# Kernel tuning notes

Measured on AMD Instinct MI355X. Metric: run time of the kernel, lower is better.

## Reference

```python
import jax, jax.numpy as jnp
import numpy as np
import math

NUM_HEADS = 16  # power of two -> simple ALiBi slope formula

def alibi_slopes(num_heads: int) -> jnp.ndarray:
    # num_heads is a power of two here; general formula per Press et al. 2022
    k = 1 << (num_heads.bit_length() - 1)
    ratio = 2.0 ** (-8.0 / k)
    slopes = ratio ** np.arange(1, 1 + k)
    if num_heads != k:
        ratio2 = 2.0 ** (-8.0 / (2 * k))
        rest = (ratio2 ** np.arange(1, 1 + 2 * k, 2))[: num_heads - k]
        slopes = np.concatenate([slopes, rest])
    return jnp.asarray(slopes, dtype=jnp.float32).reshape(1, -1, 1, 1)


def setup_inputs() -> dict:
    key = jax.random.key(0)
    kq, kk, kv, km = jax.random.split(key, 4)
    B, H, S, D = 1, NUM_HEADS, 2048, 64
    query = jax.random.normal(kq, (B, H, S, D), dtype=jnp.float32)
    k_ = jax.random.normal(kk, (B, H, S, D), dtype=jnp.float32)
    value = jax.random.normal(kv, (B, H, S, D), dtype=jnp.float32)
    # padding-style boolean mask [B, S]; keep position 0 always valid
    mask = jax.random.randint(km, (B, S), 0, 2).astype(bool)
    mask = mask.at[:, 0].set(True)
    return {"query": query, "key": k_, "value": value, "mask": mask}


def reference(query, key, value, mask):
    B, H, S, D = query.shape
    scale = 1.0 / math.sqrt(D)
    # scores: [B, H, Sq, Sk]
    scores = jnp.einsum("bhqd,bhkd->bhqk", query, key) * scale
    # causal ALiBi bias: distances arange(1-S, 1) -> shape (1, H, 1, S)
    distances = jnp.arange(1 - S, 1, dtype=jnp.float32)
    bias = distances[None, None, None, :] * alibi_slopes(H)
    scores = scores + bias
    # boolean padding mask [B, S] -> [B, 1, 1, S]
    blocked = jnp.finfo(scores.dtype).min
    scores = jnp.where(mask[:, None, None, :], scores, blocked)
    weights = jax.nn.softmax(scores, axis=-1)
    # dropout_prob = 0.0 (eval) -> identity
    return jnp.einsum("bhqk,bhkd->bhqd", weights, value)
```

## Files before the change

kernel.cpp:

```cpp
#include <hip/hip_runtime.h>


constexpr int   S_LEN  = 2048;
constexpr int   D_DIM  = 64;
constexpr int   H_NUM  = 16;
constexpr int   QT     = 128;
constexpr int   K_TILE = 64;
constexpr int   NTILE  = S_LEN / K_TILE;
constexpr int   NKS    = 4;
constexpr int   QB     = S_LEN / QT;
constexpr int   PROWSTR= 36;
constexpr float SCL    = 0.18033688f;
constexpr float L2E    = 1.44269504f;
constexpr float MASKED = -50000.0f;
constexpr float CUTOFF = 40.0f;

typedef short bf16x8 __attribute__((ext_vector_type(8)));
typedef short bf16x4 __attribute__((ext_vector_type(4)));
typedef float f32x4  __attribute__((ext_vector_type(4)));

__device__ inline short f2bf(float f) {
    union { float f; unsigned u; } x; x.f = f;
    return (short)((x.u + 0x7fffu + ((x.u >> 16) & 1u)) >> 16);
}

__device__ inline unsigned pack2bf(float a, float b) {
#if __has_builtin(__builtin_amdgcn_cvt_pk_bf16_f32)
    auto p = __builtin_amdgcn_cvt_pk_bf16_f32(a, b);
    unsigned u; __builtin_memcpy(&u, &p, 4); return u;
#else
    return (unsigned)(unsigned short)f2bf(a) | ((unsigned)(unsigned short)f2bf(b) << 16);
#endif
}

__device__ inline float fexp2(float x) {
#if __has_builtin(__builtin_amdgcn_exp2f)
    return __builtin_amdgcn_exp2f(x);
#else
    return exp2f(x);
#endif
}

__device__ inline unsigned permb(unsigned hi, unsigned lo, unsigned sel) {
#if __has_builtin(__builtin_amdgcn_perm)
    return __builtin_amdgcn_perm(hi, lo, sel);
#else
    return (sel == 0x05040100u) ? ((lo & 0xffffu) | (hi << 16))
                                : ((lo >> 16) | (hi & 0xffff0000u));
#endif
}

__device__ inline void load_lds16(const void* g, void* l) {
    __builtin_amdgcn_global_load_lds((const __attribute__((address_space(1))) void*)g,
                                     (__attribute__((address_space(3))) void*)l, 16, 0, 0);
}

__device__ inline int head_t0(int h) {
    const float slope_l2e = exp2f(-0.5f * (float)(h + 1)) * L2E;
    const float kmin = 2047.0f - CUTOFF / slope_l2e;
    return kmin <= 0.0f ? 0 : ((int)kmin) >> 6;
}

__global__ __launch_bounds__(256)
void preprocess_kernel(const float* __restrict__ Km, const float* __restrict__ Vm,
                       const void* __restrict__ maskp,
                       short* __restrict__ Kswz, short* __restrict__ Vswz,
                       float* __restrict__ Bias)
{
    __shared__ int mask_is_i32;
    const int tid = threadIdx.x;
    const int kt = blockIdx.x, h = blockIdx.y;
    if (kt < head_t0(h)) return;

    const int kbase = kt * K_TILE;
    const size_t tbase = ((size_t)h * S_LEN + kbase) * D_DIM;
    short* Kd = Kswz + ((size_t)h * NTILE + kt) * 4096;
    short* Vd = Vswz + ((size_t)h * NTILE + kt) * 4096;

    if (tid == 0) {
        const unsigned* mi = (const unsigned*)maskp;
        int ok = 1;
        for (int i = 0; i < 64; ++i) ok &= (mi[i] <= 1u);
        mask_is_i32 = ok;
    }

    #pragma unroll
    for (int it = 0; it < 2; ++it) {
        const int idx = it * 256 + tid;
        const int key = idx >> 3, c = idx & 7;
        const float* src = Km + tbase + key * 64 + c * 8;
        float4 a = *(const float4*)src;
        float4 b = *(const float4*)(src + 4);
        unsigned u[4] = { pack2bf(a.x, a.y), pack2bf(a.z, a.w),
                          pack2bf(b.x, b.y), pack2bf(b.z, b.w) };
        bf16x8 kp; __builtin_memcpy(&kp, u, 16);
        *(bf16x8*)(Kd + key * 64 + ((c ^ (key & 7)) << 3)) = kp;
    }

    {
        const int db = tid >> 4, kb = tid & 15;
        const int d4 = db * 4, key4 = kb * 4;
        float4 vv[4];
        #pragma unroll
        for (int j = 0; j < 4; ++j)
            vv[j] = *(const float4*)(Vm + tbase + (key4 + j) * 64 + d4);
        const float* vp = (const float*)vv;
        #pragma unroll
        for (int jj = 0; jj < 4; ++jj) {
            const int d = d4 + jj;
            bf16x4 ov;
            ov[0] = f2bf(vp[0 * 4 + jj]); ov[1] = f2bf(vp[1 * 4 + jj]);
            ov[2] = f2bf(vp[2 * 4 + jj]); ov[3] = f2bf(vp[3 * 4 + jj]);
            *(bf16x4*)(Vd + d * 64 + (((key4 >> 3) ^ (d & 7)) << 3) + (key4 & 7)) = ov;
        }
    }
    __syncthreads();
    if (tid < K_TILE) {
        const int key = kbase + tid;
        const int mv = mask_is_i32 ? ((const int*)maskp)[key]
                                   : (int)((const unsigned char*)maskp)[key];
        const float slope_l2e = exp2f(-0.5f * (float)(h + 1)) * L2E;
        Bias[h * S_LEN + key] = mv ? slope_l2e * (float)(key - (S_LEN - 1)) : MASKED;
    }
}

__global__ __launch_bounds__(256, 4)
void attn_main(const float* __restrict__ Qm, const short* __restrict__ Kswz,
               const short* __restrict__ Vswz, const float* __restrict__ Bias,
               float* __restrict__ Opart, float* __restrict__ lp)
{
    __shared__ short    k_lds[4096];
    __shared__ short    v_lds[4096];
    __shared__ float    bm_lds[64];
    __shared__ unsigned p_lds[4][32 * PROWSTR];

    const int tid = threadIdx.x;
    const int wave = tid >> 6, lane = tid & 63;
    const int l16 = lane & 15, quad = lane >> 4;
    const int h = blockIdx.y, qblk = blockIdx.x, ks = blockIdx.z;

    const int t0 = head_t0(h);
    const int nt = NTILE - t0;
    const int tstart = t0 + (ks * nt) / NKS;
    const int tend   = t0 + ((ks + 1) * nt) / NKS;
    if (tstart >= tend) return;

    const unsigned psel = (quad < 2) ? 0x05040100u : 0x07060302u;

    bf16x8 qfrag[2][2];
    {
        const float* Qh = Qm + (size_t)h * S_LEN * D_DIM;
        #pragma unroll
        for (int s = 0; s < 2; ++s) {
            const int qrow = qblk * QT + wave * 32 + s * 16 + l16;
            #pragma unroll
            for (int t = 0; t < 2; ++t) {
                const float* src = Qh + (size_t)qrow * D_DIM + t * 32 + quad * 8;
                float4 a = *(const float4*)src;
                float4 b = *(const float4*)(src + 4);
                unsigned* qp = (unsigned*)&qfrag[s][t];
                qp[0] = pack2bf(a.x * SCL, a.y * SCL);
                qp[1] = pack2bf(a.z * SCL, a.w * SCL);
                qp[2] = pack2bf(b.x * SCL, b.y * SCL);
                qp[3] = pack2bf(b.z * SCL, b.w * SCL);
            }
        }
    }

    bf16x8 onesv;
    #pragma unroll
    for (int i = 0; i < 8; ++i) onesv[i] = (short)0x3F80;

    f32x4 o_frag[2][4], l4[2];
    #pragma unroll
    for (int s = 0; s < 2; ++s) {
        #pragma unroll
        for (int c = 0; c < 4; ++c) o_frag[s][c] = (f32x4){0.f, 0.f, 0.f, 0.f};
        l4[s] = (f32x4){0.f, 0.f, 0.f, 0.f};
    }

    const short* Kh = Kswz + (size_t)h * NTILE * 4096;
    const short* Vh = Vswz + (size_t)h * NTILE * 4096;
    const float* Bh = Bias + h * S_LEN;
    unsigned* pw = p_lds[wave];
    const int swz = l16 & 7;

    for (int kt = tstart; kt < tend; ++kt) {
        __syncthreads();
        {
            const char* kg = (const char*)(Kh + (size_t)kt * 4096);
            const char* vg = (const char*)(Vh + (size_t)kt * 4096);
            char* kl = (char*)k_lds + wave * 2048;
            char* vl = (char*)v_lds + wave * 2048;
            const int go = wave * 2048 + lane * 16;
            load_lds16(kg + go,        kl);
            load_lds16(kg + go + 1024, kl + 1024);
            load_lds16(vg + go,        vl);
            load_lds16(vg + go + 1024, vl + 1024);
        }
        if (tid < 16) {
            float4 b4 = *(const float4*)(Bh + kt * K_TILE + tid * 4);
            *(float4*)&bm_lds[tid * 4] = b4;
        }
        __syncthreads();

        f32x4 sv[2][4];
        #pragma unroll
        for (int c = 0; c < 4; ++c) {
            const float b = bm_lds[c * 16 + l16];
            const f32x4 binit = (f32x4){b, b, b, b};
            sv[0][c] = binit;
            sv[1][c] = binit;
            #pragma unroll
            for (int t = 0; t < 2; ++t) {
                bf16x8 bfrag = *(const bf16x8*)&k_lds[(c * 16 + l16) * 64 + (((t * 4 + quad) ^ swz) << 3)];
                sv[0][c] = __builtin_amdgcn_mfma_f32_16x16x32_bf16(qfrag[0][t], bfrag, sv[0][c], 0, 0, 0);
                sv[1][c] = __builtin_amdgcn_mfma_f32_16x16x32_bf16(qfrag[1][t], bfrag, sv[1][c], 0, 0, 0);
            }
        }

        #pragma unroll
        for (int s = 0; s < 2; ++s) {
            #pragma unroll
            for (int r = 0; r < 4; ++r) {
                const float p0 = fexp2(sv[s][0][r]);
                const float p1 = fexp2(sv[s][1][r]);
                const float p2 = fexp2(sv[s][2][r]);
                const float p3 = fexp2(sv[s][3][r]);
                unsigned* pp = &pw[(s * 16 + quad * 4 + r) * PROWSTR + l16];
                pp[0]  = pack2bf(p0, p1);
                pp[16] = pack2bf(p2, p3);
            }
        }

        #pragma unroll
        for (int t2 = 0; t2 < 2; ++t2) {
            bf16x8 pfrag[2];
            #pragma unroll
            for (int s = 0; s < 2; ++s) {
                const unsigned* pr = &pw[(s * 16 + l16) * PROWSTR + t2 * 16 + (quad & 1) * 8];
                uint4 w0 = *(const uint4*)(pr);
                uint4 w1 = *(const uint4*)(pr + 4);
                unsigned pf[4];
                pf[0] = permb(w0.y, w0.x, psel);
                pf[1] = permb(w0.w, w0.z, psel);
                pf[2] = permb(w1.y, w1.x, psel);
                pf[3] = permb(w1.w, w1.z, psel);
                __builtin_memcpy(&pfrag[s], pf, 16);
            }
            #pragma unroll
            for (int c2 = 0; c2 < 4; ++c2) {
                bf16x8 vfrag = *(const bf16x8*)&v_lds[(c2 * 16 + l16) * 64 + (((t2 * 4 + quad) ^ swz) << 3)];
                o_frag[0][c2] = __builtin_amdgcn_mfma_f32_16x16x32_bf16(pfrag[0], vfrag, o_frag[0][c2], 0, 0, 0);
                o_frag[1][c2] = __builtin_amdgcn_mfma_f32_16x16x32_bf16(pfrag[1], vfrag, o_frag[1][c2], 0, 0, 0);
            }
            l4[0] = __builtin_amdgcn_mfma_f32_16x16x32_bf16(pfrag[0], onesv, l4[0], 0, 0, 0);
            l4[1] = __builtin_amdgcn_mfma_f32_16x16x32_bf16(pfrag[1], onesv, l4[1], 0, 0, 0);
        }
    }

    #pragma unroll
    for (int s = 0; s < 2; ++s) {
        const int g = qblk * 32 + wave * 8 + s * 4 + quad;
        const size_t gbase = ((size_t)ks * (H_NUM * 512) + h * 512 + g);
        #pragma unroll
        for (int c2 = 0; c2 < 4; ++c2) {
            float* dst = Opart + (gbase * 64 + c2 * 16 + l16) * 4;
            *(f32x4*)dst = o_frag[s][c2];
        }
        if (l16 == 0) *(f32x4*)(lp + gbase * 4) = l4[s];
    }
}

__global__ __launch_bounds__(256)
void attn_combine_kernel(const float* __restrict__ Opart, const float* __restrict__ lp,
                         float* __restrict__ Om)
{
    constexpr int G = H_NUM * 512;
    const int t  = blockIdx.x * 256 + threadIdx.x;
    const int gg = t >> 6;
    const int col = t & 63;
    const int h  = gg >> 9;

    const int t0 = head_t0(h);
    const int nt = NTILE - t0;

    f32x4 acc = (f32x4){0.f, 0.f, 0.f, 0.f};
    f32x4 den = (f32x4){0.f, 0.f, 0.f, 0.f};
    #pragma unroll
    for (int k = 0; k < NKS; ++k) {
        if (((k + 1) * nt) / NKS > (k * nt) / NKS) {
            const f32x4 l  = *(const f32x4*)(lp + ((size_t)k * G + gg) * 4);
            const f32x4 op = *(const f32x4*)(Opart + (((size_t)k * G + gg) * 64 + col) * 4);
            den += l;
            acc += op;
        }
    }
    #pragma unroll
    for (int r = 0; r < 4; ++r)
        Om[(size_t)(gg * 4 + r) * 64 + col] = acc[r] / den[r];
}

extern "C" void kernel_launch(void* const* d_in, const int* in_sizes, int n_in,
                              void* d_out, int out_size, void* d_ws, size_t ws_size,
                              hipStream_t stream) {
    (void)in_sizes; (void)n_in; (void)out_size; (void)ws_size;
    const float* Q = (const float*)d_in[0];
    const float* K = (const float*)d_in[1];
    const float* V = (const float*)d_in[2];
    const void*  M = d_in[3];
    float* O = (float*)d_out;

    char* ws = (char*)d_ws;
    size_t off = 0;
    short* Kswz = (short*)(ws + off); off += (size_t)H_NUM * S_LEN * D_DIM * 2;
    short* Vswz = (short*)(ws + off); off += (size_t)H_NUM * S_LEN * D_DIM * 2;
    float* Bias = (float*)(ws + off); off += (size_t)H_NUM * S_LEN * 4;
    float* Opart = (float*)(ws + off); off += (size_t)NKS * H_NUM * S_LEN * D_DIM * 4;
    float* lp   = (float*)(ws + off); off += (size_t)NKS * H_NUM * 512 * 4 * 4;

    preprocess_kernel<<<dim3(NTILE, H_NUM), 256, 0, stream>>>(K, V, M, Kswz, Vswz, Bias);
    attn_main<<<dim3(QB, H_NUM, NKS), 256, 0, stream>>>(Q, Kswz, Vswz, Bias, Opart, lp);
    attn_combine_kernel<<<(H_NUM * 512 * 64) / 256, 256, 0, stream>>>(Opart, lp, O);
}
```

Baseline: 107.6 us.

## Split key range per head adaptively and write output directly for single-chunk heads

Replaces the fixed 4-way key split with a per-head chunk count of about 4 tiles per chunk, capped at 8. This evens out work across blocks for heads whose ALiBi cutoff leaves few key tiles. Heads with a single chunk now normalise and write the final output inside the main kernel, and the combine kernel skips them. The mask-type check is also changed to use a wave ballot instead of a serial loop. In exchange, the partial-output workspace grows, and more blocks are launched that exit early.

```diff
diff --git a/kernel.cpp b/kernel.cpp
--- a/kernel.cpp
+++ b/kernel.cpp
@@ -7,7 +7,7 @@
 constexpr int   QT     = 128;
 constexpr int   K_TILE = 64;
 constexpr int   NTILE  = S_LEN / K_TILE;
-constexpr int   NKS    = 4;
+constexpr int   MAXNC  = 8;
 constexpr int   QB     = S_LEN / QT;
 constexpr int   PROWSTR= 36;
 constexpr float SCL    = 0.18033688f;
@@ -59,6 +59,11 @@
     const float slope_l2e = exp2f(-0.5f * (float)(h + 1)) * L2E;
     const float kmin = 2047.0f - CUTOFF / slope_l2e;
     return kmin <= 0.0f ? 0 : ((int)kmin) >> 6;
+}
+__device__ inline int head_nc(int h) {
+    const int nt = NTILE - head_t0(h);
+    const int nc = (nt + 3) >> 2;
+    return nc > MAXNC ? MAXNC : nc;
 }
 
 __global__ __launch_bounds__(256)
@@ -77,11 +82,10 @@
     short* Kd = Kswz + ((size_t)h * NTILE + kt) * 4096;
     short* Vd = Vswz + ((size_t)h * NTILE + kt) * 4096;
 
-    if (tid == 0) {
-        const unsigned* mi = (const unsigned*)maskp;
-        int ok = 1;
-        for (int i = 0; i < 64; ++i) ok &= (mi[i] <= 1u);
-        mask_is_i32 = ok;
+    if (tid < 64) {
+        const unsigned v = ((const unsigned*)maskp)[tid];
+        const unsigned long long b = __ballot(v <= 1u);
+        if (tid == 0) mask_is_i32 = (b == ~0ULL);
     }
 
     #pragma unroll
@@ -127,7 +131,8 @@
 __global__ __launch_bounds__(256, 4)
 void attn_main(const float* __restrict__ Qm, const short* __restrict__ Kswz,
                const short* __restrict__ Vswz, const float* __restrict__ Bias,
-               float* __restrict__ Opart, float* __restrict__ lp)
+               float* __restrict__ Om, float* __restrict__ Opart,
+               float* __restrict__ lp)
 {
     __shared__ short    k_lds[4096];
     __shared__ short    v_lds[4096];
@@ -137,13 +142,14 @@
     const int tid = threadIdx.x;
     const int wave = tid >> 6, lane = tid & 63;
     const int l16 = lane & 15, quad = lane >> 4;
-    const int h = blockIdx.y, qblk = blockIdx.x, ks = blockIdx.z;
-
+    const int h = blockIdx.y, qblk = blockIdx.x, c = blockIdx.z;
+
+    const int nc = head_nc(h);
+    if (c >= nc) return;
     const int t0 = head_t0(h);
     const int nt = NTILE - t0;
-    const int tstart = t0 + (ks * nt) / NKS;
-    const int tend   = t0 + ((ks + 1) * nt) / NKS;
-    if (tstart >= tend) return;
+    const int tstart = t0 + (c * nt) / nc;
+    const int tend   = t0 + ((c + 1) * nt) / nc;
 
     const unsigned psel = (quad < 2) ? 0x05040100u : 0x07060302u;
 
@@ -175,7 +181,7 @@
     #pragma unroll
     for (int s = 0; s < 2; ++s) {
         #pragma unroll
-        for (int c = 0; c < 4; ++c) o_frag[s][c] = (f32x4){0.f, 0.f, 0.f, 0.f};
+        for (int cc = 0; cc < 4; ++cc) o_frag[s][cc] = (f32x4){0.f, 0.f, 0.f, 0.f};
         l4[s] = (f32x4){0.f, 0.f, 0.f, 0.f};
     }
 
@@ -206,16 +212,16 @@
 
         f32x4 sv[2][4];
         #pragma unroll
-        for (int c = 0; c < 4; ++c) {
-            const float b = bm_lds[c * 16 + l16];
+        for (int cc = 0; cc < 4; ++cc) {
+            const float b = bm_lds[cc * 16 + l16];
             const f32x4 binit = (f32x4){b, b, b, b};
-            sv[0][c] = binit;
-            sv[1][c] = binit;
+            sv[0][cc] = binit;
+            sv[1][cc] = binit;
             #pragma unroll
             for (int t = 0; t < 2; ++t) {
-                bf16x8 bfrag = *(const bf16x8*)&k_lds[(c * 16 + l16) * 64 + (((t * 4 + quad) ^ swz) << 3)];
-                sv[0][c] = __builtin_amdgcn_mfma_f32_16x16x32_bf16(qfrag[0][t], bfrag, sv[0][c], 0, 0, 0);
-                sv[1][c] = __builtin_amdgcn_mfma_f32_16x16x32_bf16(qfrag[1][t], bfrag, sv[1][c], 0, 0, 0);
+                bf16x8 bfrag = *(const bf16x8*)&k_lds[(cc * 16 + l16) * 64 + (((t * 4 + quad) ^ swz) << 3)];
+                sv[0][cc] = __builtin_amdgcn_mfma_f32_16x16x32_bf16(qfrag[0][t], bfrag, sv[0][cc], 0, 0, 0);
+                sv[1][cc] = __builtin_amdgcn_mfma_f32_16x16x32_bf16(qfrag[1][t], bfrag, sv[1][cc], 0, 0, 0);
             }
         }
 
@@ -259,16 +265,34 @@
         }
     }
 
-    #pragma unroll
-    for (int s = 0; s < 2; ++s) {
-        const int g = qblk * 32 + wave * 8 + s * 4 + quad;
-        const size_t gbase = ((size_t)ks * (H_NUM * 512) + h * 512 + g);
-        #pragma unroll
-        for (int c2 = 0; c2 < 4; ++c2) {
-            float* dst = Opart + (gbase * 64 + c2 * 16 + l16) * 4;
-            *(f32x4*)dst = o_frag[s][c2];
-        }
-        if (l16 == 0) *(f32x4*)(lp + gbase * 4) = l4[s];
+    if (nc == 1) {
+        float* Oh = Om + (size_t)h * S_LEN * D_DIM;
+        const int qrow0 = qblk * QT + wave * 32;
+        #pragma unroll
+        for (int s = 0; s < 2; ++s) {
+            #pragma unroll
+            for (int r = 0; r < 4; ++r) {
+                const float inv = 1.0f / l4[s][r];
+                const int row = qrow0 + s * 16 + quad * 4 + r;
+                float* dst = Oh + (size_t)row * D_DIM + l16;
+                dst[0]  = o_frag[s][0][r] * inv;
+                dst[16] = o_frag[s][1][r] * inv;
+                dst[32] = o_frag[s][2][r] * inv;
+                dst[48] = o_frag[s][3][r] * inv;
+            }
+        }
+    } else {
+        #pragma unroll
+        for (int s = 0; s < 2; ++s) {
+            const int g = qblk * 32 + wave * 8 + s * 4 + quad;
+            const size_t gbase = (((size_t)h * MAXNC + c) * 512 + g);
+            #pragma unroll
+            for (int c2 = 0; c2 < 4; ++c2) {
+                float* dst = Opart + (gbase * 64 + c2 * 16 + l16) * 4;
+                *(f32x4*)dst = o_frag[s][c2];
+            }
+            if (l16 == 0) *(f32x4*)(lp + gbase * 4) = l4[s];
+        }
     }
 }
 
@@ -276,29 +300,25 @@
 void attn_combine_kernel(const float* __restrict__ Opart, const float* __restrict__ lp,
                          float* __restrict__ Om)
 {
-    constexpr int G = H_NUM * 512;
-    const int t  = blockIdx.x * 256 + threadIdx.x;
-    const int gg = t >> 6;
+    const int t   = blockIdx.x * 256 + threadIdx.x;
     const int col = t & 63;
-    const int h  = gg >> 9;
-
-    const int t0 = head_t0(h);
-    const int nt = NTILE - t0;
+    const int g   = (t >> 6) & 511;
+    const int h   = t >> 15;
+
+    const int nc = head_nc(h);
+    if (nc == 1) return;
 
     f32x4 acc = (f32x4){0.f, 0.f, 0.f, 0.f};
     f32x4 den = (f32x4){0.f, 0.f, 0.f, 0.f};
-    #pragma unroll
-    for (int k = 0; k < NKS; ++k) {
-        if (((k + 1) * nt) / NKS > (k * nt) / NKS) {
-            const f32x4 l  = *(const f32x4*)(lp + ((size_t)k * G + gg) * 4);
-            const f32x4 op = *(const f32x4*)(Opart + (((size_t)k * G + gg) * 64 + col) * 4);
-            den += l;
-            acc += op;
-        }
-    }
+    for (int c = 0; c < nc; ++c) {
+        const size_t gbase = (((size_t)h * MAXNC + c) * 512 + g);
+        den += *(const f32x4*)(lp + gbase * 4);
+        acc += *(const f32x4*)(Opart + (gbase * 64 + col) * 4);
+    }
+    float* Oh = Om + (size_t)h * S_LEN * D_DIM;
     #pragma unroll
     for (int r = 0; r < 4; ++r)
-        Om[(size_t)(gg * 4 + r) * 64 + col] = acc[r] / den[r];
+        Oh[(size_t)(g * 4 + r) * 64 + col] = acc[r] / den[r];
 }
 
 extern "C" void kernel_launch(void* const* d_in, const int* in_sizes, int n_in,
@@ -316,10 +336,10 @@
     short* Kswz = (short*)(ws + off); off += (size_t)H_NUM * S_LEN * D_DIM * 2;
     short* Vswz = (short*)(ws + off); off += (size_t)H_NUM * S_LEN * D_DIM * 2;
     float* Bias = (float*)(ws + off); off += (size_t)H_NUM * S_LEN * 4;
-    float* Opart = (float*)(ws + off); off += (size_t)NKS * H_NUM * S_LEN * D_DIM * 4;
-    float* lp   = (float*)(ws + off); off += (size_t)NKS * H_NUM * 512 * 4 * 4;
+    float* Opart = (float*)(ws + off); off += (size_t)H_NUM * MAXNC * 512 * 64 * 4 * 4;
+    float* lp   = (float*)(ws + off); off += (size_t)H_NUM * MAXNC * 512 * 4 * 4;
 
     preprocess_kernel<<<dim3(NTILE, H_NUM), 256, 0, stream>>>(K, V, M, Kswz, Vswz, Bias);
-    attn_main<<<dim3(QB, H_NUM, NKS), 256, 0, stream>>>(Q, Kswz, Vswz, Bias, Opart, lp);
+    attn_main<<<dim3(QB, H_NUM, MAXNC), 256, 0, stream>>>(Q, Kswz, Vswz, Bias, O, Opart, lp);
     attn_combine_kernel<<<(H_NUM * 512 * 64) / 256, 256, 0, stream>>>(Opart, lp, O);
 }
```

After: 97.89 us. -9.0%, faster.
